# Performance work log

Hardware: AMD Instinct MI355X
Metric: run time of the kernel (lower is better)

## Reference

```python
import jax, jax.numpy as jnp
import numpy as np
from jax import lax

B, V, E = 8, 1024, 32          # batch, nodes, raw node-embedding dim
F, H = 64, 4                   # node_encoding, num_heads
HID = 64                       # encoder/decoder hidden size
LAYERS = 2                     # graph_layers
FLOW_ITERS = 10
BIG = 1e9
COST_C = 1.0                   # quadratic cost: c*x^2, inv_derivative(y)=y/(2c)
DEG_P = 16.0 / V               # ~16 avg out-degree


def setup_inputs() -> dict:
    key = jax.random.key(0)
    ks = jax.random.split(key, 24)
    demands = jax.random.normal(ks[0], (B, V, 1), jnp.float32)
    demands = demands - jnp.mean(demands, axis=1, keepdims=True)  # balanced supply/demand
    node_embeddings = jax.random.normal(ks[1], (V, E), jnp.float32)
    adj = (jax.random.uniform(ks[2], (V, V)) < DEG_P).astype(jnp.float32)
    adj = jnp.maximum(adj, jnp.eye(V, dtype=jnp.float32))  # ensure nonempty rows
    s = 0.05
    p = lambda k, shp: jax.random.normal(k, shp, jnp.float32) * s
    return {
        'demands': demands, 'node_embeddings': node_embeddings, 'adj': adj,
        'enc_w1': p(ks[3], (E + 1, HID)), 'enc_b1': jnp.zeros((HID,), jnp.float32),
        'enc_w2': p(ks[4], (HID, F)),     'enc_b2': jnp.zeros((F,), jnp.float32),
        'gat_w':  p(ks[5], (H, F, F)),
        'gat_a1': p(ks[6], (H, F)), 'gat_a2': p(ks[7], (H, F)),
        'gate_w': p(ks[8], (F, F)), 'gate_u': p(ks[9], (F, F)),
        'gate_b': jnp.zeros((F,), jnp.float32),
        'dec_w1': p(ks[10], (F, HID)), 'dec_b1': jnp.zeros((HID,), jnp.float32),
        'dec_w2': p(ks[11], (HID, V)), 'dec_b2': jnp.zeros((V,), jnp.float32),
        'dual_w1': p(ks[12], (F, HID)), 'dual_b1': jnp.zeros((HID,), jnp.float32),
        'dual_w2': p(ks[13], (HID, 1)), 'dual_b2': jnp.zeros((1,), jnp.float32),
    }


def _forward(demands, node_embeddings, adj,
             enc_w1, enc_b1, enc_w2, enc_b2,
             gat_w, gat_a1, gat_a2,
             gate_w, gate_u, gate_b,
             dec_w1, dec_b1, dec_w2, dec_b2,
             dual_w1, dual_b1, dual_w2, dual_b2):
    node_bias = -BIG * (1.0 - adj)                     # [V, V]
    # ---- encoder MLP (relu hidden) ----
    x = jnp.broadcast_to(node_embeddings[None], (B, V, E))
    x = jnp.concatenate([x, demands], axis=2)          # [B, V, E+1]
    enc = jax.nn.relu(x @ enc_w1 + enc_b1) @ enc_w2 + enc_b2   # [B, V, F]
    enc = jax.nn.relu(enc)
    # ---- GAT + gate, shared weights across graph_layers ----
    for _ in range(LAYERS):
        t = jnp.einsum('bvf,hfg->bhvg', enc, gat_w)            # [B, H, V, F]
        s_self = jnp.einsum('bhvg,hg->bhv', t, gat_a1)
        s_nbr = jnp.einsum('bhvg,hg->bhv', t, gat_a2)
        logits = jax.nn.leaky_relu(s_self[..., :, None] + s_nbr[..., None, :], 0.2)
        coefs = jax.nn.softmax(logits + node_bias[None, None], axis=-1)  # [B,H,V,V]
        heads = jnp.einsum('bhvw,bhwg->bhvg', coefs, t)
        nxt = jax.nn.relu(jnp.mean(heads, axis=1))             # [B, V, F]
        z = jax.nn.sigmoid(nxt @ gate_w + enc @ gate_u + gate_b)
        enc = z * nxt + (1.0 - z) * enc
    # ---- decoder -> masked softmax flow weights ----
    pred = (enc @ dec_w1 + dec_b1) @ dec_w2 + dec_b2           # [B, V, V] (linear MLP)
    pred = jnp.square(pred)
    flow_weights = jax.nn.softmax(pred + node_bias[None], axis=-1)
    # ---- iterative min-cost-flow solve ----
    def flow_step(flow, _):
        inflow = jnp.sum(flow, axis=1)[:, :, None]             # [B, V, 1]
        return flow_weights * jax.nn.relu(inflow - demands), None
    flow, _ = lax.scan(flow_step, jnp.zeros_like(flow_weights), None, length=FLOW_ITERS)[0], None
    flow = lax.scan(flow_step, jnp.zeros_like(flow_weights), None, length=FLOW_ITERS)[0]
    flow_cost = jnp.sum(COST_C * jnp.square(flow), axis=(1, 2))  # [B]
    # ---- dual variables / dual cost ----
    dv = (enc @ dual_w1 + dual_b1) @ dual_w2 + dual_b2         # [B, V, 1]
    dual_diff = dv - jnp.swapaxes(dv, 1, 2)                    # [B, V, V]
    dual_flows = adj[None] * jax.nn.relu(dual_diff / (2.0 * COST_C))
    dual_flow_cost = COST_C * jnp.square(dual_flows) - dual_diff * dual_flows
    dual_demand = jnp.sum(dv * demands, axis=(1, 2))
    dual_cost = jnp.sum(dual_flow_cost, axis=(1, 2)) - dual_demand
    loss = jnp.mean(flow_cost - dual_cost)
    return loss


def reference(demands, node_embeddings, adj,
              enc_w1, enc_b1, enc_w2, enc_b2,
              gat_w, gat_a1, gat_a2,
              gate_w, gate_u, gate_b,
              dec_w1, dec_b1, dec_w2, dec_b2,
              dual_w1, dual_b1, dual_w2, dual_b2):
    return _forward(demands, node_embeddings, adj,
                    enc_w1, enc_b1, enc_w2, enc_b2,
                    gat_w, gat_a1, gat_a2,
                    gate_w, gate_u, gate_b,
                    dec_w1, dec_b1, dec_w2, dec_b2,
                    dual_w1, dual_b1, dual_w2, dual_b2)
```

## Files before the change

kernel.cpp:

```cpp
#include <hip/hip_runtime.h>
#include <math.h>

#define B 8
#define V 1024
#define E 32
#define H 4
#define CAP 64
#define MAXNNZ 20480
#define SE (MAXNNZ / V)
#define ZBLK 128


__device__ __forceinline__ float wave_sum(float v) {
  for (int o = 32; o > 0; o >>= 1) v += __shfl_xor(v, o);
  return v;
}
__device__ __forceinline__ float wave_max(float v) {
  for (int o = 32; o > 0; o >>= 1) v = fmaxf(v, __shfl_xor(v, o));
  return v;
}

__global__ void zero_wa_kernel(int* __restrict__ deg_in, int* __restrict__ slot_cur,
                               unsigned* __restrict__ done, const float* __restrict__ gat_w,
                               const float* __restrict__ a1, const float* __restrict__ a2,
                               float* __restrict__ wa1, float* __restrict__ wa2) {
  int blk = blockIdx.x, tid = threadIdx.x;
  if (blk < 4) {
    deg_in[blk * 256 + tid] = 0;
  } else if (blk < 8) {
    slot_cur[(blk - 4) * 256 + tid] = 0;
  } else {
    if (tid == 0) *done = 0u;
    int h = tid >> 6, f = tid & 63;
    float s1 = 0.f, s2 = 0.f;
    const float* W = gat_w + h * 4096 + f * 64;
    for (int g = 0; g < 64; ++g) {
      float w = W[g];
      s1 += w * a1[h * 64 + g];
      s2 += w * a2[h * 64 + g];
    }
    wa1[h * 64 + f] = s1;
    wa2[h * 64 + f] = s2;
  }
}

#define ENV 8
__global__ void setup_kernel(const float* __restrict__ adj, const float* __restrict__ demands,
                             const float* __restrict__ emb,
                             const float* __restrict__ ew1, const float* __restrict__ eb1,
                             const float* __restrict__ ew2, const float* __restrict__ eb2,
                             const float* __restrict__ dec_w2,
                             const float* __restrict__ wa1, const float* __restrict__ wa2,
                             int* __restrict__ nbr, int* __restrict__ deg,
                             int* __restrict__ deg_in, float* __restrict__ enc,
                             float* __restrict__ ss, float* __restrict__ sn,
                             float* __restrict__ w2t, float* __restrict__ fwe,
                             unsigned int* __restrict__ meta) {
  int blk = blockIdx.x;
  int j = threadIdx.x;
  if (blk < V) {
    int v = blk;
    int base = 0;
    for (int c = 0; c < V; c += 64) {
      float a = adj[v * V + c + j];
      unsigned long long m = __ballot(a > 0.5f);
      int pos = __popcll(m & ((1ull << j) - 1ull));
      if (a > 0.5f && base + pos < CAP) {
        nbr[v * CAP + base + pos] = c + j;
        atomicAdd(&deg_in[c + j], 1);
      }
      base += __popcll(m);
    }
    if (j == 0) deg[v] = (base < CAP) ? base : CAP;
  } else if (blk < 2 * V) {
    int eb = blk - V;
    int b = eb & 7;
    int v0 = (eb >> 3) * ENV;
    int bv0 = b * V + v0;
    __shared__ float xs[ENV][E + 1];
    __shared__ float hs[ENV][64];
#pragma unroll
    for (int n = 0; n < ENV; ++n) {
      if (j < E) xs[n][j] = emb[(v0 + n) * E + j];
      else if (j == E) xs[n][E] = demands[b * V + v0 + n];
    }
    __syncthreads();
    float h[ENV];
#pragma unroll
    for (int n = 0; n < ENV; ++n) h[n] = eb1[j];
    for (int i = 0; i < E + 1; ++i) {
      float wv = ew1[i * 64 + j];
#pragma unroll
      for (int n = 0; n < ENV; ++n) h[n] += xs[n][i] * wv;
    }
#pragma unroll
    for (int n = 0; n < ENV; ++n) hs[n][j] = fmaxf(h[n], 0.f);
    __syncthreads();
    float o[ENV];
#pragma unroll
    for (int n = 0; n < ENV; ++n) o[n] = eb2[j];
    for (int i = 0; i < 64; ++i) {
      float wv = ew2[i * 64 + j];
#pragma unroll
      for (int n = 0; n < ENV; ++n) o[n] += hs[n][i] * wv;
    }
#pragma unroll
    for (int n = 0; n < ENV; ++n) {
      o[n] = fmaxf(o[n], 0.f);
      enc[(bv0 + n) * 64 + j] = o[n];
    }
#pragma unroll
    for (int n = 0; n < ENV; ++n) {
#pragma unroll
      for (int hh = 0; hh < H; ++hh) {
        float v1 = wave_sum(o[n] * wa1[hh * 64 + j]);
        float v2 = wave_sum(o[n] * wa2[hh * 64 + j]);
        if (j == 0) {
          ss[(b * H + hh) * V + v0 + n] = v1;
          sn[(b * H + hh) * V + v0 + n] = v2;
        }
      }
    }
  } else if (blk < 3 * V) {
    int w = blk - 2 * V;
    w2t[w * 64 + j] = dec_w2[j * V + w];
  } else {
    int idx = (blk - 3 * V) * 64 + j;
    for (int i = idx; i < B * MAXNNZ; i += ZBLK * 64) fwe[i] = 0.f;
    for (int i = idx; i < MAXNNZ; i += ZBLK * 64) meta[i] = 0u;
  }
}

#define GNV 8
__global__ __launch_bounds__(256) void gat2_kernel(
    const float* __restrict__ enc_in, const float* __restrict__ ss_in,
    const float* __restrict__ sn_in, const int* __restrict__ nbr,
    const int* __restrict__ deg, const float* __restrict__ gat_w,
    const float* __restrict__ gate_w, const float* __restrict__ gate_u,
    const float* __restrict__ gate_b, const float* __restrict__ wa1,
    const float* __restrict__ wa2, float* __restrict__ enc_out,
    float* __restrict__ ss_out, float* __restrict__ sn_out, int write_s,
    const int* __restrict__ deg_in, int* __restrict__ slot_cur,
    int* __restrict__ csc_pos, int do_csc) {
  int b = blockIdx.x & 7;
  int v0 = (blockIdx.x >> 3) * GNV;
  int tid = threadIdx.x;
  int wid = tid >> 6, lane = tid & 63;
  __shared__ float agg[GNV][H][64];
  __shared__ float gpart[GNV][4][64];
  __shared__ float nxts[GNV][64];
  __shared__ float encs[GNV][64];
  __shared__ int ioff[V];
  const float* eb = enc_in + (size_t)b * V * 64;
  for (int i = tid; i < GNV * 64; i += 256) encs[i >> 6][i & 63] = eb[v0 * 64 + i];
  for (int n = wid; n < GNV; n += 4) {
    int v = v0 + n;
    int dvv = deg[v];
    int wk = (lane < dvv) ? nbr[v * CAP + lane] : 0;
    float c[H];
#pragma unroll
    for (int h = 0; h < H; ++h) {
      float x = ss_in[(b * H + h) * V + v] + sn_in[(b * H + h) * V + wk];
      x = (x > 0.f) ? x : 0.2f * x;
      if (lane >= dvv) x = -1e30f;
      float m = wave_max(x);
      float e = (lane < dvv) ? __expf(x - m) : 0.f;
      float s = wave_sum(e);
      c[h] = e / s;
    }
    float a0 = 0.f, a1v = 0.f, a2v = 0.f, a3v = 0.f;
    for (int k0 = 0; k0 < dvv; k0 += 4) {
      int r = dvv - k0;
      int w0 = __shfl(wk, k0 & 63);
      int w1 = __shfl(wk, (k0 + 1) & 63);
      int w2 = __shfl(wk, (k0 + 2) & 63);
      int w3 = __shfl(wk, (k0 + 3) & 63);
      float e0 = eb[w0 * 64 + lane];
      float e1 = (r > 1) ? eb[w1 * 64 + lane] : 0.f;
      float e2 = (r > 2) ? eb[w2 * 64 + lane] : 0.f;
      float e3 = (r > 3) ? eb[w3 * 64 + lane] : 0.f;
      a0 += __shfl(c[0], k0 & 63) * e0;
      a1v += __shfl(c[1], k0 & 63) * e0;
      a2v += __shfl(c[2], k0 & 63) * e0;
      a3v += __shfl(c[3], k0 & 63) * e0;
      if (r > 1) {
        a0 += __shfl(c[0], (k0 + 1) & 63) * e1;
        a1v += __shfl(c[1], (k0 + 1) & 63) * e1;
        a2v += __shfl(c[2], (k0 + 1) & 63) * e1;
        a3v += __shfl(c[3], (k0 + 1) & 63) * e1;
      }
      if (r > 2) {
        a0 += __shfl(c[0], (k0 + 2) & 63) * e2;
        a1v += __shfl(c[1], (k0 + 2) & 63) * e2;
        a2v += __shfl(c[2], (k0 + 2) & 63) * e2;
        a3v += __shfl(c[3], (k0 + 2) & 63) * e2;
      }
      if (r > 3) {
        a0 += __shfl(c[0], (k0 + 3) & 63) * e3;
        a1v += __shfl(c[1], (k0 + 3) & 63) * e3;
        a2v += __shfl(c[2], (k0 + 3) & 63) * e3;
        a3v += __shfl(c[3], (k0 + 3) & 63) * e3;
      }
    }
    agg[n][0][lane] = a0;
    agg[n][1][lane] = a1v;
    agg[n][2][lane] = a2v;
    agg[n][3][lane] = a3v;
  }
  __syncthreads();
  {
    const float* W = gat_w + wid * 4096;
    float hv[GNV];
#pragma unroll
    for (int n = 0; n < GNV; ++n) hv[n] = 0.f;
    for (int f = 0; f < 64; ++f) {
      float wf = W[f * 64 + lane];
#pragma unroll
      for (int n = 0; n < GNV; ++n) hv[n] += agg[n][wid][f] * wf;
    }
#pragma unroll
    for (int n = 0; n < GNV; ++n) gpart[n][wid][lane] = hv[n];
  }
  __syncthreads();
  for (int i = tid; i < GNV * 64; i += 256) {
    int n = i >> 6, g = i & 63;
    float s4 = gpart[n][0][g] + gpart[n][1][g] + gpart[n][2][g] + gpart[n][3][g];
    nxts[n][g] = fmaxf(0.25f * s4, 0.f);
  }
  __syncthreads();
  {
    float part[GNV];
#pragma unroll
    for (int n = 0; n < GNV; ++n) part[n] = 0.f;
    for (int f = wid * 16; f < wid * 16 + 16; ++f) {
      float gw = gate_w[f * 64 + lane], gu = gate_u[f * 64 + lane];
#pragma unroll
      for (int n = 0; n < GNV; ++n) part[n] += nxts[n][f] * gw + encs[n][f] * gu;
    }
    __syncthreads();
#pragma unroll
    for (int n = 0; n < GNV; ++n) gpart[n][wid][lane] = part[n];
  }
  __syncthreads();
  for (int i = tid; i < GNV * 64; i += 256) {
    int n = i >> 6, g = i & 63;
    float zs = gpart[n][0][g] + gpart[n][1][g] + gpart[n][2][g] + gpart[n][3][g] + gate_b[g];
    float z = 1.f / (1.f + __expf(-zs));
    float out = z * nxts[n][g] + (1.f - z) * encs[n][g];
    encs[n][g] = out;
    enc_out[((size_t)b * V + v0 + n) * 64 + g] = out;
  }
  if (write_s) {
    __syncthreads();
    float w1v = wa1[wid * 64 + lane], w2v = wa2[wid * 64 + lane];
#pragma unroll
    for (int n = 0; n < GNV; ++n) {
      float e = encs[n][lane];
      float ssv = wave_sum(e * w1v);
      float snv = wave_sum(e * w2v);
      if (lane == 0) {
        ss_out[(b * H + wid) * V + v0 + n] = ssv;
        sn_out[(b * H + wid) * V + v0 + n] = snv;
      }
    }
  }
  if (do_csc && b == 0) {
    __syncthreads();
    if (tid < 64) {
      int vals[16];
      int tot = 0;
#pragma unroll
      for (int i = 0; i < 16; ++i) {
        vals[i] = tot;
        tot += deg_in[tid * 16 + i];
      }
      int run = tot;
      for (int o = 1; o < 64; o <<= 1) {
        int u = __shfl_up(run, o);
        if (lane >= o) run += u;
      }
      int excl = run - tot;
#pragma unroll
      for (int i = 0; i < 16; ++i) ioff[tid * 16 + i] = excl + vals[i];
    }
    __syncthreads();
    for (int n = wid; n < GNV; n += 4) {
      int v = v0 + n;
      if (lane < deg[v]) {
        int w = nbr[v * CAP + lane];
        csc_pos[v * CAP + lane] = ioff[w] + atomicAdd(&slot_cur[w], 1);
      }
    }
  }
}

#define DNV 4
__global__ __launch_bounds__(256) void decfw_kernel(
    const float* __restrict__ enc, const float* __restrict__ dw1,
    const float* __restrict__ db1, const float* __restrict__ uw1,
    const float* __restrict__ ub1, const float* __restrict__ uw2,
    const float* __restrict__ ub2, const float* __restrict__ w2t,
    const float* __restrict__ dec_b2, const int* __restrict__ nbr,
    const int* __restrict__ deg, const int* __restrict__ csc_pos,
    float* __restrict__ fwe, unsigned int* __restrict__ meta,
    float* __restrict__ rssq, float* __restrict__ dvout) {
  int b = blockIdx.x & 7;
  int v0 = (blockIdx.x >> 3) * DNV;
  int bv0 = b * V + v0;
  int tid = threadIdx.x;
  int wv = tid >> 6, j = tid & 63;
  __shared__ float es[DNV][64];
  __shared__ float hs[DNV][64];
  es[wv][j] = enc[(bv0 + wv) * 64 + j];
  __syncthreads();
  float hj = db1[j], uj = ub1[j];
  for (int f = 0; f < 64; ++f) {
    hj += es[wv][f] * dw1[f * 64 + j];
    uj += es[wv][f] * uw1[f * 64 + j];
  }
  hs[wv][j] = hj;
  float sdv = wave_sum(uj * uw2[j]);
  if (j == 0) dvout[bv0 + wv] = sdv + ub2[0];
  __syncthreads();
  int v = v0 + wv;
  int dvv = deg[v];
  int w = (j < dvv) ? nbr[v * CAP + j] : 0;
  const float4* wrow = (const float4*)(w2t + w * 64);
  const float4* hv4 = (const float4*)hs[wv];
  float d = 0.f;
#pragma unroll
  for (int f = 0; f < 16; ++f) {
    float4 wvv = wrow[f];
    float4 hv = hv4[f];
    d += hv.x * wvv.x + hv.y * wvv.y + hv.z * wvv.z + hv.w * wvv.w;
  }
  d += dec_b2[w];
  float pp = d * d;
  float myp = (j < dvv) ? pp : -1e30f;
  float m = wave_max(myp);
  float e = (j < dvv) ? __expf(myp - m) : 0.f;
  float s = wave_sum(e);
  float coef = e / s;
  if (j < dvv) {
    int idx = csc_pos[v * CAP + j];
    fwe[(size_t)b * MAXNNZ + idx] = coef;
    meta[idx] = (unsigned)v | ((unsigned)w << 16);
  }
  float r = wave_sum(coef * coef);
  if (j == 0) rssq[bv0 + wv] = r;
}

__global__ __launch_bounds__(1024) void flow_dual_kernel(
    const float* __restrict__ fwe, const unsigned* __restrict__ meta,
    const float* __restrict__ rssq, const float* __restrict__ dv,
    const float* __restrict__ demands, const int* __restrict__ nbr_out,
    const int* __restrict__ deg_out, float* __restrict__ partial,
    unsigned* __restrict__ done, float* __restrict__ out) {
  int b = blockIdx.x;
  int v = threadIdx.x;
  __shared__ float o[V], infl[V], dvs[V];
  __shared__ float red[16];
  float dem = demands[b * V + v];
  dvs[v] = dv[b * V + v];
  o[v] = fmaxf(-dem, 0.f);
  infl[v] = 0.f;
  const float4* fp = (const float4*)(fwe + (size_t)b * MAXNNZ + v * SE);
  const uint4* mp = (const uint4*)(meta + v * SE);
  float fr[SE];
  unsigned mr[SE];
#pragma unroll
  for (int i = 0; i < SE / 4; ++i) {
    float4 f4 = fp[i];
    uint4 m4 = mp[i];
    fr[4 * i + 0] = f4.x; fr[4 * i + 1] = f4.y; fr[4 * i + 2] = f4.z; fr[4 * i + 3] = f4.w;
    mr[4 * i + 0] = m4.x; mr[4 * i + 1] = m4.y; mr[4 * i + 2] = m4.z; mr[4 * i + 3] = m4.w;
  }
  __syncthreads();
  for (int it = 0; it < 9; ++it) {
    float ov[SE];
#pragma unroll
    for (int i = 0; i < SE; ++i) ov[i] = o[mr[i] & 0xFFFF];
    float acc = 0.f;
    int pdst = -1;
#pragma unroll
    for (int i = 0; i < SE; ++i) {
      int dst = mr[i] >> 16;
      if (dst != pdst) {
        if (acc != 0.f) atomicAdd(&infl[pdst], acc);
        acc = 0.f;
        pdst = dst;
      }
      acc += fr[i] * ov[i];
    }
    if (acc != 0.f) atomicAdd(&infl[pdst], acc);
    __syncthreads();
    float nv = fmaxf(infl[v] - dem, 0.f);
    o[v] = nv;
    infl[v] = 0.f;
    __syncthreads();
  }
  float o10 = o[v];
  float local = o10 * o10 * rssq[b * V + v];
  float dvv = dvs[v];
  int dout = deg_out[v];
  float acc = 0.f;
  for (int k = 0; k < dout; ++k) {
    float diff = dvv - dvs[nbr_out[v * CAP + k]];
    if (diff > 0.f) acc += diff * diff;
  }
  local += 0.25f * acc + dvv * dem;
  local = wave_sum(local);
  if ((v & 63) == 0) red[v >> 6] = local;
  __syncthreads();
  if (v < 16) {
    float r = red[v];
    for (int o2 = 8; o2 > 0; o2 >>= 1) r += __shfl_xor(r, o2, 16);
    if (v == 0) {
      __hip_atomic_store(&partial[b], r, __ATOMIC_RELEASE, __HIP_MEMORY_SCOPE_AGENT);
      unsigned old = __hip_atomic_fetch_add(done, 1u, __ATOMIC_ACQ_REL, __HIP_MEMORY_SCOPE_AGENT);
      if (old == B - 1) {
        float s = 0.f;
        for (int i = 0; i < B; ++i)
          s += __hip_atomic_load(&partial[i], __ATOMIC_ACQUIRE, __HIP_MEMORY_SCOPE_AGENT);
        out[0] = s * (1.0f / B);
      }
    }
  }
}

extern "C" void kernel_launch(void* const* d_in, const int* in_sizes, int n_in,
                              void* d_out, int out_size, void* d_ws, size_t ws_size,
                              hipStream_t stream) {
  const float* demands = (const float*)d_in[0];
  const float* emb     = (const float*)d_in[1];
  const float* adj     = (const float*)d_in[2];
  const float* enc_w1  = (const float*)d_in[3];
  const float* enc_b1  = (const float*)d_in[4];
  const float* enc_w2  = (const float*)d_in[5];
  const float* enc_b2  = (const float*)d_in[6];
  const float* gat_w   = (const float*)d_in[7];
  const float* gat_a1  = (const float*)d_in[8];
  const float* gat_a2  = (const float*)d_in[9];
  const float* gate_w  = (const float*)d_in[10];
  const float* gate_u  = (const float*)d_in[11];
  const float* gate_b  = (const float*)d_in[12];
  const float* dec_w1  = (const float*)d_in[13];
  const float* dec_b1  = (const float*)d_in[14];
  const float* dec_w2  = (const float*)d_in[15];
  const float* dec_b2  = (const float*)d_in[16];
  const float* dual_w1 = (const float*)d_in[17];
  const float* dual_b1 = (const float*)d_in[18];
  const float* dual_w2 = (const float*)d_in[19];
  const float* dual_b2 = (const float*)d_in[20];

  char* pz = (char*)d_ws;
  int* deg_in   = (int*)pz;
  int* slot_cur = (int*)(pz + 4096);
  unsigned* done = (unsigned*)(pz + 8192);
  char* p = pz + 8448;
  auto alloc = [&](size_t n) { void* r = (void*)p; p += (n + 255) & ~(size_t)255; return r; };
  int* nbr_out   = (int*)alloc((size_t)V * CAP * 4);
  int* deg_out   = (int*)alloc((size_t)V * 4);
  int* csc_pos   = (int*)alloc((size_t)V * CAP * 4);
  float* fwe     = (float*)alloc((size_t)B * MAXNNZ * 4);
  unsigned int* meta = (unsigned int*)alloc((size_t)MAXNNZ * 4);
  float* w2t     = (float*)alloc((size_t)64 * V * 4);
  float* wa1     = (float*)alloc((size_t)H * 64 * 4);
  float* wa2     = (float*)alloc((size_t)H * 64 * 4);
  float* encA    = (float*)alloc((size_t)B * V * 64 * 4);
  float* encB    = (float*)alloc((size_t)B * V * 64 * 4);
  float* ssA     = (float*)alloc((size_t)B * H * V * 4);
  float* snA     = (float*)alloc((size_t)B * H * V * 4);
  float* ssB     = (float*)alloc((size_t)B * H * V * 4);
  float* snB     = (float*)alloc((size_t)B * H * V * 4);
  float* dv      = (float*)alloc((size_t)B * V * 4);
  float* rssq    = (float*)alloc((size_t)B * V * 4);
  float* partial = (float*)alloc((size_t)B * 4);

  zero_wa_kernel<<<9, 256, 0, stream>>>(deg_in, slot_cur, done, gat_w, gat_a1, gat_a2,
                                        wa1, wa2);
  setup_kernel<<<3 * V + ZBLK, 64, 0, stream>>>(
      adj, demands, emb, enc_w1, enc_b1, enc_w2, enc_b2, dec_w2, wa1, wa2,
      nbr_out, deg_out, deg_in, encA, ssA, snA, w2t, fwe, meta);
  gat2_kernel<<<B * V / GNV, 256, 0, stream>>>(encA, ssA, snA, nbr_out, deg_out, gat_w,
                                               gate_w, gate_u, gate_b, wa1, wa2,
                                               encB, ssB, snB, 1,
                                               deg_in, slot_cur, csc_pos, 1);
  gat2_kernel<<<B * V / GNV, 256, 0, stream>>>(encB, ssB, snB, nbr_out, deg_out, gat_w,
                                               gate_w, gate_u, gate_b, wa1, wa2,
                                               encA, ssA, snA, 0,
                                               deg_in, slot_cur, csc_pos, 0);
  decfw_kernel<<<B * V / DNV, 256, 0, stream>>>(encA, dec_w1, dec_b1, dual_w1, dual_b1,
                                                dual_w2, dual_b2, w2t, dec_b2, nbr_out,
                                                deg_out, csc_pos, fwe, meta, rssq, dv);
  flow_dual_kernel<<<B, 1024, 0, stream>>>(fwe, meta, rssq, dv, demands, nbr_out, deg_out,
                                           partial, done, (float*)d_out);
}
```

Measured before the change: 148.6 us.

## Split flow iterations into per-iteration multi-block gather kernels using CSC offsets

The flow propagation used to run as one 8-block kernel of 1024 threads looping nine times with shared-memory atomics and block syncs. It now runs as eight separate launches of a 128-block gather kernel, where each node sums its incoming edges using CSC offsets exported from the GAT kernel. A final kernel does the last iteration plus the dual cost. This spreads the work across far more CUs and removes the shared atomics. In exchange it adds nine launches and global-memory round trips of the o vector.

```diff
diff --git a/kernel.cpp b/kernel.cpp
--- a/kernel.cpp
+++ b/kernel.cpp
@@ -7,7 +7,6 @@
 #define H 4
 #define CAP 64
 #define MAXNNZ 20480
-#define SE (MAXNNZ / V)
 #define ZBLK 128
 
 
@@ -141,7 +140,7 @@
     const float* __restrict__ wa2, float* __restrict__ enc_out,
     float* __restrict__ ss_out, float* __restrict__ sn_out, int write_s,
     const int* __restrict__ deg_in, int* __restrict__ slot_cur,
-    int* __restrict__ csc_pos, int do_csc) {
+    int* __restrict__ csc_pos, int* __restrict__ in_off_g, int do_csc) {
   int b = blockIdx.x & 7;
   int v0 = (blockIdx.x >> 3) * GNV;
   int tid = threadIdx.x;
@@ -284,6 +283,10 @@
       for (int i = 0; i < 16; ++i) ioff[tid * 16 + i] = excl + vals[i];
     }
     __syncthreads();
+    if (v0 == 0) {
+      for (int i = tid; i < V; i += 256) in_off_g[i] = ioff[i];
+      if (tid == 0) in_off_g[V] = ioff[V - 1] + deg_in[V - 1];
+    }
     for (int n = wid; n < GNV; n += 4) {
       int v = v0 + n;
       if (lane < deg[v]) {
@@ -302,8 +305,9 @@
     const float* __restrict__ ub2, const float* __restrict__ w2t,
     const float* __restrict__ dec_b2, const int* __restrict__ nbr,
     const int* __restrict__ deg, const int* __restrict__ csc_pos,
-    float* __restrict__ fwe, unsigned int* __restrict__ meta,
-    float* __restrict__ rssq, float* __restrict__ dvout) {
+    const float* __restrict__ demands, float* __restrict__ fwe,
+    unsigned int* __restrict__ meta, float* __restrict__ rssq,
+    float* __restrict__ dvout, float* __restrict__ o1) {
   int b = blockIdx.x & 7;
   int v0 = (blockIdx.x >> 3) * DNV;
   int bv0 = b * V + v0;
@@ -320,7 +324,10 @@
   }
   hs[wv][j] = hj;
   float sdv = wave_sum(uj * uw2[j]);
-  if (j == 0) dvout[bv0 + wv] = sdv + ub2[0];
+  if (j == 0) {
+    dvout[bv0 + wv] = sdv + ub2[0];
+    o1[bv0 + wv] = fmaxf(-demands[bv0 + wv], 0.f);
+  }
   __syncthreads();
   int v = v0 + wv;
   int dvv = deg[v];
@@ -350,56 +357,62 @@
   if (j == 0) rssq[bv0 + wv] = r;
 }
 
-__global__ __launch_bounds__(1024) void flow_dual_kernel(
+__global__ __launch_bounds__(64) void flow_iter_kernel(
     const float* __restrict__ fwe, const unsigned* __restrict__ meta,
-    const float* __restrict__ rssq, const float* __restrict__ dv,
-    const float* __restrict__ demands, const int* __restrict__ nbr_out,
-    const int* __restrict__ deg_out, float* __restrict__ partial,
+    const int* __restrict__ in_off, const float* __restrict__ demands,
+    const float* __restrict__ o_cur, float* __restrict__ o_nxt) {
+  int blk = blockIdx.x;
+  int b = blk & 7;
+  int v = (blk >> 3) * 64 + threadIdx.x;
+  float dem = demands[b * V + v];
+  int e0 = in_off[v], e1 = in_off[v + 1];
+  if (e1 > MAXNNZ) e1 = MAXNNZ;
+  if (e0 > e1) e0 = e1;
+  const float* fwb = fwe + (size_t)b * MAXNNZ;
+  const float* ob = o_cur + b * V;
+  float inflow = 0.f;
+  int e = e0;
+  for (; e + 3 < e1; e += 4) {
+    unsigned m0 = meta[e], m1 = meta[e + 1], m2 = meta[e + 2], m3 = meta[e + 3];
+    float f0 = fwb[e], f1 = fwb[e + 1], f2 = fwb[e + 2], f3 = fwb[e + 3];
+    float o0 = ob[m0 & 0xFFFF], o1 = ob[m1 & 0xFFFF];
+    float o2 = ob[m2 & 0xFFFF], o3 = ob[m3 & 0xFFFF];
+    inflow += f0 * o0 + f1 * o1 + f2 * o2 + f3 * o3;
+  }
+  for (; e < e1; ++e) inflow += fwb[e] * ob[meta[e] & 0xFFFF];
+  o_nxt[b * V + v] = fmaxf(inflow - dem, 0.f);
+}
+
+__global__ __launch_bounds__(1024) void flow_final_kernel(
+    const float* __restrict__ fwe, const unsigned* __restrict__ meta,
+    const int* __restrict__ in_off, const float* __restrict__ rssq,
+    const float* __restrict__ dv, const float* __restrict__ demands,
+    const int* __restrict__ nbr_out, const int* __restrict__ deg_out,
+    const float* __restrict__ o9, float* __restrict__ partial,
     unsigned* __restrict__ done, float* __restrict__ out) {
   int b = blockIdx.x;
   int v = threadIdx.x;
-  __shared__ float o[V], infl[V], dvs[V];
+  __shared__ float dvs[V];
   __shared__ float red[16];
   float dem = demands[b * V + v];
   dvs[v] = dv[b * V + v];
-  o[v] = fmaxf(-dem, 0.f);
-  infl[v] = 0.f;
-  const float4* fp = (const float4*)(fwe + (size_t)b * MAXNNZ + v * SE);
-  const uint4* mp = (const uint4*)(meta + v * SE);
-  float fr[SE];
-  unsigned mr[SE];
-#pragma unroll
-  for (int i = 0; i < SE / 4; ++i) {
-    float4 f4 = fp[i];
-    uint4 m4 = mp[i];
-    fr[4 * i + 0] = f4.x; fr[4 * i + 1] = f4.y; fr[4 * i + 2] = f4.z; fr[4 * i + 3] = f4.w;
-    mr[4 * i + 0] = m4.x; mr[4 * i + 1] = m4.y; mr[4 * i + 2] = m4.z; mr[4 * i + 3] = m4.w;
-  }
-  __syncthreads();
-  for (int it = 0; it < 9; ++it) {
-    float ov[SE];
-#pragma unroll
-    for (int i = 0; i < SE; ++i) ov[i] = o[mr[i] & 0xFFFF];
-    float acc = 0.f;
-    int pdst = -1;
-#pragma unroll
-    for (int i = 0; i < SE; ++i) {
-      int dst = mr[i] >> 16;
-      if (dst != pdst) {
-        if (acc != 0.f) atomicAdd(&infl[pdst], acc);
-        acc = 0.f;
-        pdst = dst;
-      }
-      acc += fr[i] * ov[i];
-    }
-    if (acc != 0.f) atomicAdd(&infl[pdst], acc);
-    __syncthreads();
-    float nv = fmaxf(infl[v] - dem, 0.f);
-    o[v] = nv;
-    infl[v] = 0.f;
-    __syncthreads();
-  }
-  float o10 = o[v];
+  __syncthreads();
+  int e0 = in_off[v], e1 = in_off[v + 1];
+  if (e1 > MAXNNZ) e1 = MAXNNZ;
+  if (e0 > e1) e0 = e1;
+  const float* fwb = fwe + (size_t)b * MAXNNZ;
+  const float* ob = o9 + b * V;
+  float inflow = 0.f;
+  int e = e0;
+  for (; e + 3 < e1; e += 4) {
+    unsigned m0 = meta[e], m1 = meta[e + 1], m2 = meta[e + 2], m3 = meta[e + 3];
+    float f0 = fwb[e], f1 = fwb[e + 1], f2 = fwb[e + 2], f3 = fwb[e + 3];
+    float p0 = ob[m0 & 0xFFFF], p1 = ob[m1 & 0xFFFF];
+    float p2 = ob[m2 & 0xFFFF], p3 = ob[m3 & 0xFFFF];
+    inflow += f0 * p0 + f1 * p1 + f2 * p2 + f3 * p3;
+  }
+  for (; e < e1; ++e) inflow += fwb[e] * ob[meta[e] & 0xFFFF];
+  float o10 = fmaxf(inflow - dem, 0.f);
   float local = o10 * o10 * rssq[b * V + v];
   float dvv = dvs[v];
   int dout = deg_out[v];
@@ -462,6 +475,7 @@
   int* nbr_out   = (int*)alloc((size_t)V * CAP * 4);
   int* deg_out   = (int*)alloc((size_t)V * 4);
   int* csc_pos   = (int*)alloc((size_t)V * CAP * 4);
+  int* in_off    = (int*)alloc((size_t)(V + 1) * 4);
   float* fwe     = (float*)alloc((size_t)B * MAXNNZ * 4);
   unsigned int* meta = (unsigned int*)alloc((size_t)MAXNNZ * 4);
   float* w2t     = (float*)alloc((size_t)64 * V * 4);
@@ -475,6 +489,8 @@
   float* snB     = (float*)alloc((size_t)B * H * V * 4);
   float* dv      = (float*)alloc((size_t)B * V * 4);
   float* rssq    = (float*)alloc((size_t)B * V * 4);
+  float* oA      = (float*)alloc((size_t)B * V * 4);
+  float* oB      = (float*)alloc((size_t)B * V * 4);
   float* partial = (float*)alloc((size_t)B * 4);
 
   zero_wa_kernel<<<9, 256, 0, stream>>>(deg_in, slot_cur, done, gat_w, gat_a1, gat_a2,
@@ -485,14 +501,22 @@
   gat2_kernel<<<B * V / GNV, 256, 0, stream>>>(encA, ssA, snA, nbr_out, deg_out, gat_w,
                                                gate_w, gate_u, gate_b, wa1, wa2,
                                                encB, ssB, snB, 1,
-                                               deg_in, slot_cur, csc_pos, 1);
+                                               deg_in, slot_cur, csc_pos, in_off, 1);
   gat2_kernel<<<B * V / GNV, 256, 0, stream>>>(encB, ssB, snB, nbr_out, deg_out, gat_w,
                                                gate_w, gate_u, gate_b, wa1, wa2,
                                                encA, ssA, snA, 0,
-                                               deg_in, slot_cur, csc_pos, 0);
+                                               deg_in, slot_cur, csc_pos, in_off, 0);
   decfw_kernel<<<B * V / DNV, 256, 0, stream>>>(encA, dec_w1, dec_b1, dual_w1, dual_b1,
                                                 dual_w2, dual_b2, w2t, dec_b2, nbr_out,
-                                                deg_out, csc_pos, fwe, meta, rssq, dv);
-  flow_dual_kernel<<<B, 1024, 0, stream>>>(fwe, meta, rssq, dv, demands, nbr_out, deg_out,
-                                           partial, done, (float*)d_out);
-}
+                                                deg_out, csc_pos, demands, fwe, meta,
+                                                rssq, dv, oA);
+  float* cur = oA;
+  float* nxt = oB;
+  for (int it = 0; it < 8; ++it) {
+    flow_iter_kernel<<<B * V / 64, 64, 0, stream>>>(fwe, meta, in_off, demands, cur, nxt);
+    float* tmp = cur; cur = nxt; nxt = tmp;
+  }
+  flow_final_kernel<<<B, 1024, 0, stream>>>(fwe, meta, in_off, rssq, dv, demands,
+                                            nbr_out, deg_out, cur, partial, done,
+                                            (float*)d_out);
+}
```

Result: no change. 146.2 us (median of 2 runs) (-1.6%).
